# Kernel optimization log

Measured on AMD Instinct MI355X. Metric: run time of the kernel, lower is better.

The kernel has to match this reference:

```python
import jax, jax.numpy as jnp
import numpy as np

B, IN, H, OUT = 4096, 1024, 1024, 1024


def setup_inputs() -> dict:
    key = jax.random.key(0)
    ks = jax.random.split(key, 16)
    s_in = 1.0 / np.sqrt(IN)
    s_h = 1.0 / np.sqrt(H)
    d = {}
    d['input_vec'] = jax.random.normal(ks[0], (B, IN), jnp.float32)
    d['hidden_vec'] = jax.random.normal(ks[1], (B, H), jnp.float32)
    d['cell_vec'] = jax.random.normal(ks[2], (B, H), jnp.float32)
    names = ['f', 'i', 'o', 'g']
    for j, n in enumerate(names):
        d['Wx_' + n] = jax.random.uniform(ks[3 + 3 * j], (H, IN), jnp.float32, -s_in, s_in)
        d['bx_' + n] = jax.random.uniform(ks[4 + 3 * j], (H,), jnp.float32, -s_in, s_in)
        d['Wh_' + n] = jax.random.uniform(ks[5 + 3 * j], (H, H), jnp.float32, -s_h, s_h)
    d['W_out'] = jax.random.uniform(ks[15], (OUT, H), jnp.float32, -s_h, s_h)
    d['b_out'] = jax.random.uniform(jax.random.fold_in(key, 99), (OUT,), jnp.float32, -s_h, s_h)
    return d


def reference(input_vec, hidden_vec, cell_vec,
              Wx_f, bx_f, Wh_f,
              Wx_i, bx_i, Wh_i,
              Wx_o, bx_o, Wh_o,
              Wx_g, bx_g, Wh_g,
              W_out, b_out):
    # Fuse the 8 small linears into two GEMMs: [B,IN]x[IN,4H] and [B,H]x[H,4H].
    Wx = jnp.concatenate([Wx_f, Wx_i, Wx_o, Wx_g], axis=0)   # [4H, IN]
    Wh = jnp.concatenate([Wh_f, Wh_i, Wh_o, Wh_g], axis=0)   # [4H, H]
    b = jnp.concatenate([bx_f, bx_i, bx_o, bx_g], axis=0)    # [4H]
    gates = input_vec @ Wx.T + hidden_vec @ Wh.T + b          # [B, 4H]
    f, i, o, g = jnp.split(gates, 4, axis=1)
    f = jax.nn.sigmoid(f)
    i = jax.nn.sigmoid(i)
    o = jax.nn.sigmoid(o)
    g = jnp.tanh(g)
    new_cell = f * cell_vec + i * g
    new_hidden = o * jnp.tanh(new_cell)
    output_vec = new_hidden @ W_out.T + b_out
    return (new_hidden, new_cell, output_vec)
```

## Files before the change

kernel.cpp:

```cpp
#include <hip/hip_runtime.h>
#include <hip/hip_bf16.h>
#include <stdint.h>

#define B_   4096
#define IN_  1024
#define H_   1024
#define OUT_ 1024

typedef __attribute__((ext_vector_type(8)))  short short8;
typedef __attribute__((ext_vector_type(16))) float floatx16;

__device__ static inline void gload_lds16(const void* g, void* l) {
    __builtin_amdgcn_global_load_lds(
        (const __attribute__((address_space(1))) unsigned int*)g,
        (__attribute__((address_space(3))) unsigned int*)l,
        16, 0, 0);
}

__device__ static inline float sigmoidf_(float x) { return 1.0f / (1.0f + __expf(-x)); }
__device__ static inline float tanhf_(float x)    { return 1.0f - 2.0f / (1.0f + __expf(2.0f * x)); }

struct Ptrs8 { const float* p[8]; };

__global__ void cvt_all_kernel(const float* __restrict__ x, const float* __restrict__ h,
                               Ptrs8 ptrs, const float* __restrict__ wout,
                               __hip_bfloat16* __restrict__ xh,
                               __hip_bfloat16* __restrict__ Wc,
                               __hip_bfloat16* __restrict__ Wob) {
    int blk = blockIdx.x;
    const float* src;
    __hip_bfloat16* dst;
    if (blk < 8192) {
        int idx = blk * 256 + threadIdx.x;
        int b  = idx >> 9;
        int c4 = (idx & 511) * 4;
        src = (c4 < IN_) ? (x + (size_t)b * IN_ + c4)
                         : (h + (size_t)b * H_ + (c4 - IN_));
        dst = xh + (size_t)b * 2048 + c4;
    } else if (blk < 16384) {
        int idx = (blk - 8192) * 256 + threadIdx.x;
        int n  = idx >> 9;
        int c4 = (idx & 511) * 4;
        int gate = (n >> 5) & 3;
        int hh   = ((n >> 7) << 5) + (n & 31);
        src = (c4 < 1024) ? (ptrs.p[2 * gate]     + (size_t)hh * 1024 + c4)
                          : (ptrs.p[2 * gate + 1] + (size_t)hh * 1024 + (c4 - 1024));
        dst = Wc + (size_t)n * 2048 + c4;
    } else {
        int idx = (blk - 16384) * 256 + threadIdx.x;
        src = wout + (size_t)idx * 4;
        dst = Wob + (size_t)idx * 4;
    }
    float4 v = *(const float4*)src;
    dst[0] = __float2bfloat16(v.x);
    dst[1] = __float2bfloat16(v.y);
    dst[2] = __float2bfloat16(v.z);
    dst[3] = __float2bfloat16(v.w);
}

__global__ __launch_bounds__(256, 2) void gemm_gate_fused(
    const __hip_bfloat16* __restrict__ A,
    const __hip_bfloat16* __restrict__ Bm,
    const float* __restrict__ cell,
    const float* __restrict__ bxf, const float* __restrict__ bxi,
    const float* __restrict__ bxo, const float* __restrict__ bxg,
    float* __restrict__ new_hidden, float* __restrict__ new_cell,
    __hip_bfloat16* __restrict__ hb)
{
    constexpr int BK = 64;
    constexpr int K  = 2048;

    __shared__ __hip_bfloat16 ldsA[256 * BK];
    __shared__ __hip_bfloat16 ldsB[128 * BK];

    const int tid  = threadIdx.x;
    const int lane = tid & 63;
    const int wv   = tid >> 6;

    const int bid    = blockIdx.x;
    const int xcd    = bid & 7;
    const int loc    = bid >> 3;
    const int n_tile = xcd * 4 + (loc & 3);
    const int m_tile = loc >> 2;
    const int m0 = m_tile * 256;
    const int n0 = n_tile * 128;

    const int srow   = tid >> 3;
    const int schunk = tid & 7;
    const int scg    = schunk ^ (srow & 7);
    const __hip_bfloat16* Ag = A  + (size_t)(m0 + srow) * K + scg * 8;
    const __hip_bfloat16* Bg = Bm + (size_t)(n0 + srow) * K + scg * 8;
    char* lA = (char*)ldsA + wv * 1024;
    char* lB = (char*)ldsB + wv * 1024;

    const int wrow  = wv * 64;
    const int fr    = lane & 31;
    const int khalf = lane >> 5;

    floatx16 acc[2][4] = {};

    for (int k0 = 0; k0 < K; k0 += BK) {
        #pragma unroll
        for (int s = 0; s < 8; ++s)
            gload_lds16(Ag + (size_t)(s * 32) * K + k0, lA + s * 4096);
        #pragma unroll
        for (int s = 0; s < 4; ++s)
            gload_lds16(Bg + (size_t)(s * 32) * K + k0, lB + s * 4096);
        __syncthreads();

        #pragma unroll
        for (int kk = 0; kk < 4; ++kk) {
            const int cg = kk * 2 + khalf;
            short8 af[2], bf[4];
            #pragma unroll
            for (int i = 0; i < 2; ++i) {
                const int r = wrow + i * 32 + fr;
                af[i] = *(const short8*)((const char*)ldsA + r * 128 + ((cg ^ (r & 7)) * 16));
            }
            #pragma unroll
            for (int j = 0; j < 4; ++j) {
                const int r = j * 32 + fr;
                bf[j] = *(const short8*)((const char*)ldsB + r * 128 + ((cg ^ (r & 7)) * 16));
            }
            #pragma unroll
            for (int i = 0; i < 2; ++i)
                #pragma unroll
                for (int j = 0; j < 4; ++j)
                    acc[i][j] = __builtin_amdgcn_mfma_f32_32x32x16_bf16(af[i], bf[j], acc[i][j], 0, 0, 0);
        }
        __syncthreads();
    }

    const int h  = (n0 >> 2) + fr;
    const float bfb = bxf[h];
    const float bib = bxi[h];
    const float bob = bxo[h];
    const float bgb = bxg[h];

    #pragma unroll
    for (int i = 0; i < 2; ++i) {
        const int row_base = m0 + wrow + i * 32 + 4 * khalf;
        #pragma unroll
        for (int reg = 0; reg < 16; ++reg) {
            const int row = row_base + (reg & 3) + 8 * (reg >> 2);
            const size_t off = (size_t)row * H_ + h;
            const float f = sigmoidf_(acc[i][0][reg] + bfb);
            const float ii = sigmoidf_(acc[i][1][reg] + bib);
            const float o = sigmoidf_(acc[i][2][reg] + bob);
            const float g = tanhf_(acc[i][3][reg] + bgb);
            const float c = f * cell[off] + ii * g;
            const float nh = o * tanhf_(c);
            new_cell[off]   = c;
            new_hidden[off] = nh;
            hb[off] = __float2bfloat16(nh);
        }
    }
}

__global__ __launch_bounds__(256, 2) void gemm_out(
    const __hip_bfloat16* __restrict__ A,
    const __hip_bfloat16* __restrict__ Bm,
    float* __restrict__ C,
    const float* __restrict__ bias)
{
    constexpr int BK = 64;
    constexpr int K  = 1024;
    constexpr int N  = 1024;

    __shared__ __hip_bfloat16 ldsA[128 * BK];
    __shared__ __hip_bfloat16 ldsB[64 * BK];

    const int tid  = threadIdx.x;
    const int lane = tid & 63;
    const int wv   = tid >> 6;

    const int bid    = blockIdx.x;
    const int xcd    = bid & 7;
    const int loc    = bid >> 3;
    const int n_tile = xcd * 2 + (loc & 1);
    const int m_tile = loc >> 1;
    const int m0 = m_tile * 128;
    const int n0 = n_tile * 64;

    const int srow   = tid >> 3;
    const int schunk = tid & 7;
    const int scg    = schunk ^ (srow & 7);
    const __hip_bfloat16* Ag = A  + (size_t)(m0 + srow) * K + scg * 8;
    const __hip_bfloat16* Bg = Bm + (size_t)(n0 + srow) * K + scg * 8;
    char* lA = (char*)ldsA + wv * 1024;
    char* lB = (char*)ldsB + wv * 1024;

    const int wrow  = wv * 32;
    const int fr    = lane & 31;
    const int khalf = lane >> 5;

    floatx16 acc[2] = {};

    for (int k0 = 0; k0 < K; k0 += BK) {
        #pragma unroll
        for (int s = 0; s < 4; ++s)
            gload_lds16(Ag + (size_t)(s * 32) * K + k0, lA + s * 4096);
        #pragma unroll
        for (int s = 0; s < 2; ++s)
            gload_lds16(Bg + (size_t)(s * 32) * K + k0, lB + s * 4096);
        __syncthreads();

        #pragma unroll
        for (int kk = 0; kk < 4; ++kk) {
            const int cg = kk * 2 + khalf;
            const int ra = wrow + fr;
            short8 af = *(const short8*)((const char*)ldsA + ra * 128 + ((cg ^ (ra & 7)) * 16));
            short8 bf[2];
            #pragma unroll
            for (int j = 0; j < 2; ++j) {
                const int r = j * 32 + fr;
                bf[j] = *(const short8*)((const char*)ldsB + r * 128 + ((cg ^ (r & 7)) * 16));
            }
            #pragma unroll
            for (int j = 0; j < 2; ++j)
                acc[j] = __builtin_amdgcn_mfma_f32_32x32x16_bf16(af, bf[j], acc[j], 0, 0, 0);
        }
        __syncthreads();
    }

    #pragma unroll
    for (int j = 0; j < 2; ++j) {
        const int col = n0 + j * 32 + fr;
        const float bb = bias[col];
        #pragma unroll
        for (int reg = 0; reg < 16; ++reg) {
            const int row = m0 + wrow + 4 * khalf + (reg & 3) + 8 * (reg >> 2);
            C[(size_t)row * N + col] = acc[j][reg] + bb;
        }
    }
}

extern "C" void kernel_launch(void* const* d_in, const int* in_sizes, int n_in,
                              void* d_out, int out_size, void* d_ws, size_t ws_size,
                              hipStream_t stream) {
    const float* input_vec  = (const float*)d_in[0];
    const float* hidden_vec = (const float*)d_in[1];
    const float* cell_vec   = (const float*)d_in[2];
    const float* Wx_f = (const float*)d_in[3];
    const float* bx_f = (const float*)d_in[4];
    const float* Wh_f = (const float*)d_in[5];
    const float* Wx_i = (const float*)d_in[6];
    const float* bx_i = (const float*)d_in[7];
    const float* Wh_i = (const float*)d_in[8];
    const float* Wx_o = (const float*)d_in[9];
    const float* bx_o = (const float*)d_in[10];
    const float* Wh_o = (const float*)d_in[11];
    const float* Wx_g = (const float*)d_in[12];
    const float* bx_g = (const float*)d_in[13];
    const float* Wh_g = (const float*)d_in[14];
    const float* W_out = (const float*)d_in[15];
    const float* b_out = (const float*)d_in[16];

    char* ws = (char*)d_ws;
    __hip_bfloat16* xh  = (__hip_bfloat16*)(ws);
    __hip_bfloat16* Wc  = (__hip_bfloat16*)(ws + (16ull << 20));
    __hip_bfloat16* Wob = (__hip_bfloat16*)(ws + (32ull << 20));
    __hip_bfloat16* hb  = (__hip_bfloat16*)(ws + (34ull << 20));

    float* new_hidden = (float*)d_out;
    float* new_cell   = new_hidden + (size_t)B_ * H_;
    float* out_vec    = new_cell + (size_t)B_ * H_;

    Ptrs8 p;
    p.p[0] = Wx_f; p.p[1] = Wh_f; p.p[2] = Wx_i; p.p[3] = Wh_i;
    p.p[4] = Wx_o; p.p[5] = Wh_o; p.p[6] = Wx_g; p.p[7] = Wh_g;
    cvt_all_kernel<<<17408, 256, 0, stream>>>(input_vec, hidden_vec, p, W_out, xh, Wc, Wob);

    gemm_gate_fused<<<512, 256, 0, stream>>>(
        xh, Wc, cell_vec, bx_f, bx_i, bx_o, bx_g, new_hidden, new_cell, hb);

    gemm_out<<<512, 256, 0, stream>>>(hb, Wob, out_vec, b_out);
}
```

Before: 240.4 us.

## Double-buffer gate GEMM LDS with 256x256 tiles and 8-wave blocks

Restructures the fused gate GEMM to use 512-thread blocks computing 256x256 output tiles. Shared memory is double-buffered (128KB) so global-to-LDS loads for the next K step overlap the MFMAs on the current one, with s_setprio raising priority around the MFMA bursts. This aims to hide load latency and raise data reuse per block. In exchange it adds extra barriers per K sub-step and limits occupancy through the large LDS footprint, and the grid shrinks to 256 blocks.

```diff
diff --git a/kernel.cpp b/kernel.cpp
--- a/kernel.cpp
+++ b/kernel.cpp
@@ -58,7 +58,7 @@
     dst[3] = __float2bfloat16(v.w);
 }
 
-__global__ __launch_bounds__(256, 2) void gemm_gate_fused(
+__global__ __launch_bounds__(512, 2) void gemm_gate_fused(
     const __hip_bfloat16* __restrict__ A,
     const __hip_bfloat16* __restrict__ Bm,
     const float* __restrict__ cell,
@@ -67,71 +67,106 @@
     float* __restrict__ new_hidden, float* __restrict__ new_cell,
     __hip_bfloat16* __restrict__ hb)
 {
-    constexpr int BK = 64;
-    constexpr int K  = 2048;
-
-    __shared__ __hip_bfloat16 ldsA[256 * BK];
-    __shared__ __hip_bfloat16 ldsB[128 * BK];
+    constexpr int K = 2048;
+
+    __shared__ short lds_s[2 * 32768];
 
     const int tid  = threadIdx.x;
     const int lane = tid & 63;
     const int wv   = tid >> 6;
+    const int wr   = wv >> 1;
+    const int wc   = wv & 1;
 
     const int bid    = blockIdx.x;
     const int xcd    = bid & 7;
     const int loc    = bid >> 3;
-    const int n_tile = xcd * 4 + (loc & 3);
-    const int m_tile = loc >> 2;
+    const int n_tile = xcd * 2 + (loc & 1);
+    const int m_tile = loc >> 1;
     const int m0 = m_tile * 256;
-    const int n0 = n_tile * 128;
+    const int n0 = n_tile * 256;
 
     const int srow   = tid >> 3;
     const int schunk = tid & 7;
     const int scg    = schunk ^ (srow & 7);
     const __hip_bfloat16* Ag = A  + (size_t)(m0 + srow) * K + scg * 8;
     const __hip_bfloat16* Bg = Bm + (size_t)(n0 + srow) * K + scg * 8;
-    char* lA = (char*)ldsA + wv * 1024;
-    char* lB = (char*)ldsB + wv * 1024;
-
-    const int wrow  = wv * 64;
+
+    char* const lds = (char*)lds_s;
+    const int wvoff = wv * 1024;
+
     const int fr    = lane & 31;
     const int khalf = lane >> 5;
+    const int sw    = fr & 7;
+
+    int offA[2], offB[4];
+    #pragma unroll
+    for (int i = 0; i < 2; ++i) offA[i] = (wr * 64 + i * 32 + fr) * 128;
+    #pragma unroll
+    for (int j = 0; j < 4; ++j) offB[j] = 32768 + (wc * 128 + j * 32 + fr) * 128;
 
     floatx16 acc[2][4] = {};
 
-    for (int k0 = 0; k0 < K; k0 += BK) {
-        #pragma unroll
-        for (int s = 0; s < 8; ++s)
-            gload_lds16(Ag + (size_t)(s * 32) * K + k0, lA + s * 4096);
-        #pragma unroll
-        for (int s = 0; s < 4; ++s)
-            gload_lds16(Bg + (size_t)(s * 32) * K + k0, lB + s * 4096);
-        __syncthreads();
+    #pragma unroll
+    for (int s = 0; s < 4; ++s)
+        gload_lds16(Ag + (size_t)(s * 64) * K, lds + s * 8192 + wvoff);
+    #pragma unroll
+    for (int s = 0; s < 4; ++s)
+        gload_lds16(Bg + (size_t)(s * 64) * K, lds + 32768 + s * 8192 + wvoff);
+    asm volatile("s_waitcnt vmcnt(0)" ::: "memory");
+    __builtin_amdgcn_s_barrier();
+    __builtin_amdgcn_sched_barrier(0);
+
+    int cur = 0;
+    for (int t = 0; t < 32; ++t) {
+        char* const rb = lds + cur * 65536;
+        char* const wb = lds + (cur ^ 1) * 65536;
+        const __hip_bfloat16* Agt = Ag + (size_t)(t + 1) * 64;
+        const __hip_bfloat16* Bgt = Bg + (size_t)(t + 1) * 64;
+        const bool stage = (t < 31);
 
         #pragma unroll
         for (int kk = 0; kk < 4; ++kk) {
-            const int cg = kk * 2 + khalf;
-            short8 af[2], bf[4];
-            #pragma unroll
-            for (int i = 0; i < 2; ++i) {
-                const int r = wrow + i * 32 + fr;
-                af[i] = *(const short8*)((const char*)ldsA + r * 128 + ((cg ^ (r & 7)) * 16));
+            const int co = ((kk * 2 + khalf) ^ sw) * 16;
+            short8 af[2], bfr[4];
+            #pragma unroll
+            for (int i = 0; i < 2; ++i)
+                af[i] = *(const short8*)(rb + offA[i] + co);
+            #pragma unroll
+            for (int j = 0; j < 4; ++j)
+                bfr[j] = *(const short8*)(rb + offB[j] + co);
+
+            if (stage) {
+                if (kk == 0) {
+                    gload_lds16(Agt,                    wb + 0 * 8192 + wvoff);
+                    gload_lds16(Agt + (size_t)64 * K,   wb + 1 * 8192 + wvoff);
+                    gload_lds16(Bgt,                    wb + 32768 + 0 * 8192 + wvoff);
+                    gload_lds16(Bgt + (size_t)64 * K,   wb + 32768 + 1 * 8192 + wvoff);
+                } else if (kk == 1) {
+                    gload_lds16(Agt + (size_t)128 * K,  wb + 2 * 8192 + wvoff);
+                    gload_lds16(Agt + (size_t)192 * K,  wb + 3 * 8192 + wvoff);
+                    gload_lds16(Bgt + (size_t)128 * K,  wb + 32768 + 2 * 8192 + wvoff);
+                    gload_lds16(Bgt + (size_t)192 * K,  wb + 32768 + 3 * 8192 + wvoff);
+                }
             }
-            #pragma unroll
-            for (int j = 0; j < 4; ++j) {
-                const int r = j * 32 + fr;
-                bf[j] = *(const short8*)((const char*)ldsB + r * 128 + ((cg ^ (r & 7)) * 16));
-            }
+
+            __builtin_amdgcn_s_barrier();
+            __builtin_amdgcn_s_setprio(1);
             #pragma unroll
             for (int i = 0; i < 2; ++i)
                 #pragma unroll
                 for (int j = 0; j < 4; ++j)
-                    acc[i][j] = __builtin_amdgcn_mfma_f32_32x32x16_bf16(af[i], bf[j], acc[i][j], 0, 0, 0);
+                    acc[i][j] = __builtin_amdgcn_mfma_f32_32x32x16_bf16(af[i], bfr[j], acc[i][j], 0, 0, 0);
+            __builtin_amdgcn_s_setprio(0);
+            if (kk == 3)
+                asm volatile("s_waitcnt vmcnt(0)" ::: "memory");
+            __builtin_amdgcn_s_barrier();
+            if (kk == 3)
+                __builtin_amdgcn_sched_barrier(0);
         }
-        __syncthreads();
-    }
-
-    const int h  = (n0 >> 2) + fr;
+        cur ^= 1;
+    }
+
+    const int h  = ((n0 + wc * 128) >> 2) + fr;
     const float bfb = bxf[h];
     const float bib = bxi[h];
     const float bob = bxo[h];
@@ -139,16 +174,16 @@
 
     #pragma unroll
     for (int i = 0; i < 2; ++i) {
-        const int row_base = m0 + wrow + i * 32 + 4 * khalf;
+        const int row_base = m0 + wr * 64 + i * 32 + 4 * khalf;
         #pragma unroll
         for (int reg = 0; reg < 16; ++reg) {
             const int row = row_base + (reg & 3) + 8 * (reg >> 2);
             const size_t off = (size_t)row * H_ + h;
-            const float f = sigmoidf_(acc[i][0][reg] + bfb);
+            const float f  = sigmoidf_(acc[i][0][reg] + bfb);
             const float ii = sigmoidf_(acc[i][1][reg] + bib);
-            const float o = sigmoidf_(acc[i][2][reg] + bob);
-            const float g = tanhf_(acc[i][3][reg] + bgb);
-            const float c = f * cell[off] + ii * g;
+            const float o  = sigmoidf_(acc[i][2][reg] + bob);
+            const float g  = tanhf_(acc[i][3][reg] + bgb);
+            const float c  = f * cell[off] + ii * g;
             const float nh = o * tanhf_(c);
             new_cell[off]   = c;
             new_hidden[off] = nh;
@@ -271,7 +306,7 @@
     p.p[4] = Wx_o; p.p[5] = Wh_o; p.p[6] = Wx_g; p.p[7] = Wh_g;
     cvt_all_kernel<<<17408, 256, 0, stream>>>(input_vec, hidden_vec, p, W_out, xh, Wc, Wob);
 
-    gemm_gate_fused<<<512, 256, 0, stream>>>(
+    gemm_gate_fused<<<256, 512, 0, stream>>>(
         xh, Wc, cell_vec, bx_f, bx_i, bx_o, bx_g, new_hidden, new_cell, hb);
 
     gemm_out<<<512, 256, 0, stream>>>(hb, Wob, out_vec, b_out);
```

Result: slower. 245.3 us (+2.0%).
